# Kernel optimization log

Measured on AMD Instinct MI355X. Metric: run time of the kernel, lower is better.

The kernel has to match this reference:

```python
import jax, jax.numpy as jnp
import numpy as np

NEG_INF = np.float32(-np.inf)

def setup_inputs() -> dict:
    key = jax.random.key(0)
    k1, k2 = jax.random.split(key)
    x = jax.random.normal(k1, (8, 4, 512, 512), dtype=jnp.float32)
    weight = jax.random.normal(k2, (8, 4, 5, 5), dtype=jnp.float32)
    return {"x": x, "weight": weight}

def reference(x, weight):
    # Morphological (max-plus) dilation:
    # out[n,co,h,w] = max_{ci,kh,kw} x[n,ci,h+kh-oh, w+kw-ow] + weight[co,ci,kh,kw]
    # origin (oh,ow) = kernel_size // 2; out-of-bounds -> padding_value (-inf).
    N, Ci, H, W = x.shape
    Co, _, Kh, Kw = weight.shape
    oh, ow = Kh // 2, Kw // 2
    xp = jnp.pad(x, ((0, 0), (0, 0), (oh, Kh - 1 - oh), (ow, Kw - 1 - ow)),
                 constant_values=NEG_INF)
    out = jnp.full((N, Co, H, W), NEG_INF, dtype=x.dtype)
    # small fixed loop over the Kh*Kw structuring-element taps; data dims vectorized
    for kh in range(Kh):
        for kw in range(Kw):
            win = xp[:, :, kh:kh + H, kw:kw + W]            # [N,Ci,H,W]
            w_tap = weight[:, :, kh, kw]                     # [Co,Ci]
            cand = jnp.max(win[:, None] + w_tap[None, :, :, None, None], axis=2)  # [N,Co,H,W]
            out = jnp.maximum(out, cand)
    return out
```

## Files before the change

kernel.cpp:

```cpp
#include <hip/hip_runtime.h>

#define NEG_INF (-__builtin_inff())

static __device__ __forceinline__ float max3f(float a, float b, float c) {
    float d;
    asm("v_max3_f32 %0, %1, %2, %3" : "=v"(d) : "v"(a), "v"(b), "v"(c));
    return d;
}

__global__ __launch_bounds__(256, 4) void dil2d_kernel(const float* __restrict__ x,
                                                       const float* __restrict__ w,
                                                       float* __restrict__ out) {
    const int Ci = 4, H = 512, W = 512;

    const int tid = threadIdx.x;
    const int wg  = tid & 63;
    const int w0  = wg << 3;
    const int co0 = __builtin_amdgcn_readfirstlane((tid >> 6) << 1);
    const int b   = blockIdx.x;
    const int n   = b >> 9;
    const int h   = b & 511;

    float acc[2][8];
#pragma unroll
    for (int cs = 0; cs < 2; ++cs)
#pragma unroll
        for (int j = 0; j < 8; ++j) acc[cs][j] = NEG_INF;

    const float* xn = x + n * (Ci * H * W);

    const bool lo_edge = (w0 == 0);
    const bool hi_edge = (w0 == 504);
    const int  off_lo  = lo_edge ? 0   : (w0 - 4);
    const int  off_hi  = hi_edge ? 504 : (w0 + 8);

#pragma unroll
    for (int ci = 0; ci < Ci; ++ci) {
        const float* xc  = xn + ci * (H * W);
        const float* wci = w + (co0 * Ci + ci) * 25;
#pragma unroll
        for (int kh = 0; kh < 5; ++kh) {
            const int r = h + kh - 2;
            if (r < 0 || r >= H) continue;
            const float* xr = xc + r * W;

            const float4 lo4 = *(const float4*)(xr + off_lo);
            const float4 m0  = *(const float4*)(xr + w0);
            const float4 m1  = *(const float4*)(xr + w0 + 4);
            const float4 hi4 = *(const float4*)(xr + off_hi);

            float xv[12];
            xv[0]  = lo_edge ? NEG_INF : lo4.z;
            xv[1]  = lo_edge ? NEG_INF : lo4.w;
            xv[2]  = m0.x; xv[3] = m0.y; xv[4] = m0.z; xv[5] = m0.w;
            xv[6]  = m1.x; xv[7] = m1.y; xv[8] = m1.z; xv[9] = m1.w;
            xv[10] = hi_edge ? NEG_INF : hi4.x;
            xv[11] = hi_edge ? NEG_INF : hi4.y;

            const float* wk = wci + kh * 5;
#pragma unroll
            for (int cs = 0; cs < 2; ++cs) {
                const float* wco = wk + cs * (Ci * 25);
                const float wv0 = wco[0], wv1 = wco[1], wv2 = wco[2],
                            wv3 = wco[3], wv4 = wco[4];
#pragma unroll
                for (int j = 0; j < 8; ++j) {
                    const float t0 = xv[j]     + wv0;
                    const float t1 = xv[j + 1] + wv1;
                    const float t2 = xv[j + 2] + wv2;
                    const float t3 = xv[j + 3] + wv3;
                    const float t4 = xv[j + 4] + wv4;
                    float m = acc[cs][j];
                    m = max3f(m, t0, t1);
                    m = max3f(m, t2, t3);
                    m = fmaxf(m, t4);
                    acc[cs][j] = m;
                }
            }
        }
    }

    float* on = out + n * (8 * H * W) + co0 * (H * W) + h * W + w0;
#pragma unroll
    for (int cs = 0; cs < 2; ++cs) {
        float* o = on + cs * (H * W);
        *(float4*)(o)     = make_float4(acc[cs][0], acc[cs][1], acc[cs][2], acc[cs][3]);
        *(float4*)(o + 4) = make_float4(acc[cs][4], acc[cs][5], acc[cs][6], acc[cs][7]);
    }
}

extern "C" void kernel_launch(void* const* d_in, const int* in_sizes, int n_in,
                              void* d_out, int out_size, void* d_ws, size_t ws_size,
                              hipStream_t stream) {
    const float* x = (const float*)d_in[0];
    const float* w = (const float*)d_in[1];
    float* out     = (float*)d_out;

    dim3 grid(4096), block(256);
    hipLaunchKernelGGL(dil2d_kernel, grid, block, 0, stream, x, w, out);
}
```

Baseline: 143.0 us.

## Compute four output channels per thread over two rows per block with paired taps

New measurement: 133.7 us. 6.5% less time.

```diff
diff --git a/kernel.cpp b/kernel.cpp
--- a/kernel.cpp
+++ b/kernel.cpp
@@ -8,6 +8,22 @@
     return d;
 }
 
+static __device__ __forceinline__ void load_win(const float* __restrict__ xr,
+                                                int w0, int off_lo, int off_hi,
+                                                bool lo_edge, bool hi_edge,
+                                                float* xv) {
+    const float4 lo4 = *(const float4*)(xr + off_lo);
+    const float4 m0  = *(const float4*)(xr + w0);
+    const float4 m1  = *(const float4*)(xr + w0 + 4);
+    const float4 hi4 = *(const float4*)(xr + off_hi);
+    xv[0]  = lo_edge ? NEG_INF : lo4.z;
+    xv[1]  = lo_edge ? NEG_INF : lo4.w;
+    xv[2]  = m0.x; xv[3] = m0.y; xv[4] = m0.z; xv[5] = m0.w;
+    xv[6]  = m1.x; xv[7] = m1.y; xv[8] = m1.z; xv[9] = m1.w;
+    xv[10] = hi_edge ? NEG_INF : hi4.x;
+    xv[11] = hi_edge ? NEG_INF : hi4.y;
+}
+
 __global__ __launch_bounds__(256, 4) void dil2d_kernel(const float* __restrict__ x,
                                                        const float* __restrict__ w,
                                                        float* __restrict__ out) {
@@ -16,65 +32,97 @@
     const int tid = threadIdx.x;
     const int wg  = tid & 63;
     const int w0  = wg << 3;
-    const int co0 = __builtin_amdgcn_readfirstlane((tid >> 6) << 1);
+    const int coh = (tid >> 6) & 1;
+    const int rib = tid >> 7;
+    const int co0 = __builtin_amdgcn_readfirstlane(coh << 2);
     const int b   = blockIdx.x;
-    const int n   = b >> 9;
-    const int h   = b & 511;
+    const int wkid = ((b & 7) << 8) | (b >> 3);
+    const int n   = wkid >> 8;
+    const int h   = ((wkid & 255) << 1) + rib;
 
-    float acc[2][8];
+    float acc[4][8];
 #pragma unroll
-    for (int cs = 0; cs < 2; ++cs)
+    for (int cs = 0; cs < 4; ++cs)
 #pragma unroll
         for (int j = 0; j < 8; ++j) acc[cs][j] = NEG_INF;
 
     const float* xn = x + n * (Ci * H * W);
+    const float* wb = w + co0 * (Ci * 25);
 
     const bool lo_edge = (w0 == 0);
     const bool hi_edge = (w0 == 504);
     const int  off_lo  = lo_edge ? 0   : (w0 - 4);
     const int  off_hi  = hi_edge ? 504 : (w0 + 8);
 
+    if (h >= 2 && h <= 509) {
 #pragma unroll
-    for (int ci = 0; ci < Ci; ++ci) {
-        const float* xc  = xn + ci * (H * W);
-        const float* wci = w + (co0 * Ci + ci) * 25;
+        for (int p = 0; p < 10; ++p) {
+            const int gA = 2 * p, gB = 2 * p + 1;
+            const int ciA = gA / 5, khA = gA % 5;
+            const int ciB = gB / 5, khB = gB % 5;
+
+            float xa[12], xb[12];
+            load_win(xn + ciA * (H * W) + (h + khA - 2) * W,
+                     w0, off_lo, off_hi, lo_edge, hi_edge, xa);
+            load_win(xn + ciB * (H * W) + (h + khB - 2) * W,
+                     w0, off_lo, off_hi, lo_edge, hi_edge, xb);
+
+            const float* wA = wb + ciA * 25 + khA * 5;
+            const float* wB = wb + ciB * 25 + khB * 5;
 #pragma unroll
-        for (int kh = 0; kh < 5; ++kh) {
-            const int r = h + kh - 2;
-            if (r < 0 || r >= H) continue;
-            const float* xr = xc + r * W;
-
-            const float4 lo4 = *(const float4*)(xr + off_lo);
-            const float4 m0  = *(const float4*)(xr + w0);
-            const float4 m1  = *(const float4*)(xr + w0 + 4);
-            const float4 hi4 = *(const float4*)(xr + off_hi);
-
-            float xv[12];
-            xv[0]  = lo_edge ? NEG_INF : lo4.z;
-            xv[1]  = lo_edge ? NEG_INF : lo4.w;
-            xv[2]  = m0.x; xv[3] = m0.y; xv[4] = m0.z; xv[5] = m0.w;
-            xv[6]  = m1.x; xv[7] = m1.y; xv[8] = m1.z; xv[9] = m1.w;
-            xv[10] = hi_edge ? NEG_INF : hi4.x;
-            xv[11] = hi_edge ? NEG_INF : hi4.y;
-
-            const float* wk = wci + kh * 5;
-#pragma unroll
-            for (int cs = 0; cs < 2; ++cs) {
-                const float* wco = wk + cs * (Ci * 25);
-                const float wv0 = wco[0], wv1 = wco[1], wv2 = wco[2],
-                            wv3 = wco[3], wv4 = wco[4];
+            for (int cs = 0; cs < 4; ++cs) {
+                const float wa0 = wA[cs*100+0], wa1 = wA[cs*100+1], wa2 = wA[cs*100+2],
+                            wa3 = wA[cs*100+3], wa4 = wA[cs*100+4];
+                const float wb0 = wB[cs*100+0], wb1 = wB[cs*100+1], wb2 = wB[cs*100+2],
+                            wb3 = wB[cs*100+3], wb4 = wB[cs*100+4];
 #pragma unroll
                 for (int j = 0; j < 8; ++j) {
-                    const float t0 = xv[j]     + wv0;
-                    const float t1 = xv[j + 1] + wv1;
-                    const float t2 = xv[j + 2] + wv2;
-                    const float t3 = xv[j + 3] + wv3;
-                    const float t4 = xv[j + 4] + wv4;
+                    const float a0 = xa[j]     + wa0;
+                    const float a1 = xa[j + 1] + wa1;
+                    const float a2 = xa[j + 2] + wa2;
+                    const float a3 = xa[j + 3] + wa3;
+                    const float a4 = xa[j + 4] + wa4;
+                    const float b0 = xb[j]     + wb0;
+                    const float b1 = xb[j + 1] + wb1;
+                    const float b2 = xb[j + 2] + wb2;
+                    const float b3 = xb[j + 3] + wb3;
+                    const float b4 = xb[j + 4] + wb4;
                     float m = acc[cs][j];
-                    m = max3f(m, t0, t1);
-                    m = max3f(m, t2, t3);
-                    m = fmaxf(m, t4);
+                    m = max3f(m, a0, a1);
+                    m = max3f(m, a2, a3);
+                    m = max3f(m, a4, b0);
+                    m = max3f(m, b1, b2);
+                    m = max3f(m, b3, b4);
                     acc[cs][j] = m;
+                }
+            }
+        }
+    } else {
+        for (int ci = 0; ci < Ci; ++ci) {
+            for (int kh = 0; kh < 5; ++kh) {
+                const int r = h + kh - 2;
+                if (r < 0 || r >= H) continue;
+                float xv[12];
+                load_win(xn + ci * (H * W) + r * W,
+                         w0, off_lo, off_hi, lo_edge, hi_edge, xv);
+                const float* wk = wb + ci * 25 + kh * 5;
+#pragma unroll
+                for (int cs = 0; cs < 4; ++cs) {
+                    const float wv0 = wk[cs*100+0], wv1 = wk[cs*100+1], wv2 = wk[cs*100+2],
+                                wv3 = wk[cs*100+3], wv4 = wk[cs*100+4];
+#pragma unroll
+                    for (int j = 0; j < 8; ++j) {
+                        const float t0 = xv[j]     + wv0;
+                        const float t1 = xv[j + 1] + wv1;
+                        const float t2 = xv[j + 2] + wv2;
+                        const float t3 = xv[j + 3] + wv3;
+                        const float t4 = xv[j + 4] + wv4;
+                        float m = acc[cs][j];
+                        m = max3f(m, t0, t1);
+                        m = max3f(m, t2, t3);
+                        m = fmaxf(m, t4);
+                        acc[cs][j] = m;
+                    }
                 }
             }
         }
@@ -82,7 +130,7 @@
 
     float* on = out + n * (8 * H * W) + co0 * (H * W) + h * W + w0;
 #pragma unroll
-    for (int cs = 0; cs < 2; ++cs) {
+    for (int cs = 0; cs < 4; ++cs) {
         float* o = on + cs * (H * W);
         *(float4*)(o)     = make_float4(acc[cs][0], acc[cs][1], acc[cs][2], acc[cs][3]);
         *(float4*)(o + 4) = make_float4(acc[cs][4], acc[cs][5], acc[cs][6], acc[cs][7]);
@@ -96,6 +144,6 @@
     const float* w = (const float*)d_in[1];
     float* out     = (float*)d_out;
 
-    dim3 grid(4096), block(256);
+    dim3 grid(2048), block(256);
     hipLaunchKernelGGL(dil2d_kernel, grid, block, 0, stream, x, w, out);
 }
```
